# Optimization experiments

Measured on AMD Instinct MI355X. Metric: run time of the kernel, lower is better.

Reference implementation:

```python
import jax, jax.numpy as jnp
import numpy as np

KNN_K = 16
EPS = 1e-5


def _knn_idx(p, k):
    # p: [B,3,N] -> idx [B,N,k] of nearest neighbors (self excluded)
    pt = jnp.swapaxes(p, 1, 2)                      # [B,N,3]
    xx = jnp.sum(pt * pt, axis=-1)                  # [B,N]
    inner = jnp.einsum('bnd,bmd->bnm', pt, pt)      # [B,N,N]
    dist = -(xx[:, :, None] - 2.0 * inner + xx[:, None, :])  # -||pi-pj||^2
    N = pt.shape[1]
    dist = dist - 1e9 * jnp.eye(N, dtype=dist.dtype)
    return jax.lax.top_k(dist, k)[1]


def _ln(x, g, b):
    mu = jnp.mean(x, axis=-1, keepdims=True)
    var = jnp.mean((x - mu) ** 2, axis=-1, keepdims=True)
    return (x - mu) * jax.lax.rsqrt(var + EPS) * g + b


_gather = jax.vmap(lambda a, i: a[i])  # a:[N,C], i:[N,k] -> [N,k,C]


def setup_inputs() -> dict:
    key = jax.random.key(0)
    ks = jax.random.split(key, 24)
    Cin, C, B, N = 64, 128, 8, 2048
    s = lambda k_, shp, fan: jax.random.normal(k_, shp, jnp.float32) * (1.0 / np.sqrt(fan))
    return {
        'x': jax.random.normal(ks[0], (B, Cin, N), jnp.float32),
        'p': jax.random.normal(ks[1], (B, 3, N), jnp.float32),
        'Win': s(ks[2], (C, Cin), Cin), 'bin_': jnp.zeros((C,), jnp.float32),
        'Wq': s(ks[3], (C, C), C), 'Wk': s(ks[4], (C, C), C), 'Wv': s(ks[5], (C, C), C),
        'Wd1': s(ks[6], (C, 3), 3), 'bd1': jnp.zeros((C,), jnp.float32),
        'Wd2': s(ks[7], (C, C), C), 'bd2': jnp.zeros((C,), jnp.float32),
        'Wa': s(ks[8], (C, C), C), 'ba': jnp.zeros((C,), jnp.float32),
        'g1': jnp.ones((C,), jnp.float32), 'b1': jnp.zeros((C,), jnp.float32),
        'g2': jnp.ones((C,), jnp.float32), 'b2': jnp.zeros((C,), jnp.float32),
        'Wf1': s(ks[9], (4 * C, C), C), 'bf1': jnp.zeros((4 * C,), jnp.float32),
        'Wf2': s(ks[10], (C, 4 * C), 4 * C), 'bf2': jnp.zeros((C,), jnp.float32),
    }


def reference(x, p, Win, bin_, Wq, Wk, Wv, Wd1, bd1, Wd2, bd2, Wa, ba,
              g1, b1, g2, b2, Wf1, bf1, Wf2, bf2) -> jnp.ndarray:
    B, _, N = x.shape
    k = min(KNN_K, max(1, N - 1))
    # in_proj (conv1x1 == per-point linear); work in [B,N,C]
    h = jnp.einsum('oc,bcn->bno', Win, x) + bin_          # [B,N,C]
    hn = _ln(h, g1, b1)
    idx = _knn_idx(p, k)                                  # [B,N,k] (int)
    q = hn @ Wq.T                                         # [B,N,C]
    k_all = hn @ Wk.T
    v_all = hn @ Wv.T
    k_j = _gather(k_all, idx)                             # [B,N,k,C]
    v_j = _gather(v_all, idx)
    pt = jnp.swapaxes(p, 1, 2)                            # [B,N,3]
    p_j = _gather(pt, idx)                                # [B,N,k,3]
    rel = pt[:, :, None, :] - p_j                         # [B,N,k,3]
    d = jax.nn.relu(rel @ Wd1.T + bd1) @ Wd2.T + bd2      # [B,N,k,C]
    logits = (q[:, :, None, :] - k_j + d) @ Wa.T + ba     # [B,N,k,C]
    a = jax.nn.softmax(logits, axis=2)                    # softmax over neighbors
    y = jnp.sum(a * (v_j + d), axis=2)                    # [B,N,C]
    h = h + y
    h2 = _ln(h, g2, b2)
    h = h + jax.nn.relu(h2 @ Wf1.T + bf1) @ Wf2.T + bf2
    return jnp.swapaxes(h, 1, 2)                          # [B,C,N]
```

## Files before the change

kernel.cpp:

```cpp
#include <hip/hip_runtime.h>

typedef __bf16 bf16_t;
typedef __bf16 bf16x8 __attribute__((ext_vector_type(8)));
typedef __bf16 bf16x2 __attribute__((ext_vector_type(2)));
typedef float  f32x4  __attribute__((ext_vector_type(4)));

#define MFMA16(a,b,c) __builtin_amdgcn_mfma_f32_16x16x32_bf16((a),(b),(c),0,0,0)

#define BB 8
#define NN 2048
#define CC 128
#define CIN 64
#define KNB 16
#define BNT (BB*NN)

static __device__ __forceinline__ int remap256(int x) { return ((x & 7) << 5) | (x >> 3); }

static __device__ __forceinline__ bf16x8 cvt8(const float* src) {
  f32x4 a0 = *(const f32x4*)src;
  f32x4 a1 = *(const f32x4*)(src + 4);
  bf16x8 fr;
  fr[0] = (__bf16)a0[0]; fr[1] = (__bf16)a0[1]; fr[2] = (__bf16)a0[2]; fr[3] = (__bf16)a0[3];
  fr[4] = (__bf16)a1[0]; fr[5] = (__bf16)a1[1]; fr[6] = (__bf16)a1[2]; fr[7] = (__bf16)a1[3];
  return fr;
}

__global__ __launch_bounds__(256) void inproj_ln_k(
    const float* __restrict__ x, const float* __restrict__ Win, const float* __restrict__ bin,
    const float* __restrict__ g1, const float* __restrict__ b1,
    float* __restrict__ h, bf16_t* __restrict__ hnb) {
  __shared__ bf16_t As[64 * 72];
  __shared__ bf16_t Bs[128 * 72];
  __shared__ float hs[64 * 132];
  int t = threadIdx.x;
  int lane = t & 63, w = t >> 6, quad = lane >> 4, l15 = lane & 15;
  int mBase = remap256(blockIdx.x) * 64;
  int b = mBase >> 11, n0 = mBase & (NN - 1);
  const float* xb = x + (size_t)b * CIN * NN;
  {
    int k = t >> 2, part = t & 3;
    #pragma unroll
    for (int i = 0; i < 4; ++i) {
      f32x4 v = *(const f32x4*)(xb + (size_t)k * NN + n0 + part * 16 + i * 4);
      #pragma unroll
      for (int j2 = 0; j2 < 4; ++j2) As[(part * 16 + i * 4 + j2) * 72 + k] = (__bf16)v[j2];
    }
  }
  {
    int row = t >> 1, seg = (t & 1) * 32;
    #pragma unroll
    for (int i = 0; i < 4; ++i)
      *(bf16x8*)(&Bs[row * 72 + seg + i * 8]) = cvt8(Win + (size_t)row * CIN + seg + i * 8);
  }
  __syncthreads();
  f32x4 acc[2][4] = {};
  #pragma unroll
  for (int s = 0; s < 2; ++s) {
    bf16x8 af[4];
    #pragma unroll
    for (int mt = 0; mt < 4; ++mt)
      af[mt] = *(const bf16x8*)(&As[(mt * 16 + l15) * 72 + s * 32 + quad * 8]);
    #pragma unroll
    for (int t2 = 0; t2 < 2; ++t2) {
      bf16x8 bfr = *(const bf16x8*)(&Bs[((w * 2 + t2) * 16 + l15) * 72 + s * 32 + quad * 8]);
      #pragma unroll
      for (int mt = 0; mt < 4; ++mt) acc[t2][mt] = MFMA16(af[mt], bfr, acc[t2][mt]);
    }
  }
  #pragma unroll
  for (int t2 = 0; t2 < 2; ++t2) {
    int col = (w * 2 + t2) * 16 + l15;
    float bv = bin[col];
    #pragma unroll
    for (int mt = 0; mt < 4; ++mt)
      #pragma unroll
      for (int reg = 0; reg < 4; ++reg)
        hs[(mt * 16 + quad * 4 + reg) * 132 + col] = acc[t2][mt][reg] + bv;
  }
  __syncthreads();
  {
    int row = t >> 2, c0 = (t & 3) * 32;
    float v[32];
    #pragma unroll
    for (int i = 0; i < 8; ++i) *(f32x4*)(v + i * 4) = *(const f32x4*)(&hs[row * 132 + c0 + i * 4]);
    float s1 = 0.f, s2 = 0.f;
    #pragma unroll
    for (int i = 0; i < 32; ++i) { s1 += v[i]; s2 += v[i] * v[i]; }
    s1 += __shfl_xor(s1, 1); s1 += __shfl_xor(s1, 2);
    s2 += __shfl_xor(s2, 1); s2 += __shfl_xor(s2, 2);
    float mu = s1 * (1.f / CC);
    float var = s2 * (1.f / CC) - mu * mu;
    float rs = rsqrtf(var + 1e-5f);
    float* hrow = h + (size_t)(mBase + row) * CC + c0;
    #pragma unroll
    for (int i = 0; i < 8; ++i) *(f32x4*)(hrow + i * 4) = *(const f32x4*)(v + i * 4);
    bf16_t* hnrow = hnb + (size_t)(mBase + row) * CC + c0;
    #pragma unroll
    for (int i = 0; i < 4; ++i) {
      f32x4 g4a = ((const f32x4*)g1)[(c0 >> 2) + i * 2],     g4b = ((const f32x4*)g1)[(c0 >> 2) + i * 2 + 1];
      f32x4 b4a = ((const f32x4*)b1)[(c0 >> 2) + i * 2],     b4b = ((const f32x4*)b1)[(c0 >> 2) + i * 2 + 1];
      bf16x8 o;
      #pragma unroll
      for (int j = 0; j < 4; ++j) o[j]     = (__bf16)((v[i * 8 + j]     - mu) * rs * g4a[j] + b4a[j]);
      #pragma unroll
      for (int j = 0; j < 4; ++j) o[4 + j] = (__bf16)((v[i * 8 + 4 + j] - mu) * rs * g4b[j] + b4b[j]);
      *(bf16x8*)(hnrow + i * 8) = o;
    }
  }
}

static __device__ __forceinline__ void cas(double& a, double& b) {
  double lo = fmin(a, b), hi = fmax(a, b); a = lo; b = hi;
}
#define S8(K,o) \
  cas(K[o+0],K[o+1]); cas(K[o+2],K[o+3]); cas(K[o+4],K[o+5]); cas(K[o+6],K[o+7]); \
  cas(K[o+0],K[o+2]); cas(K[o+1],K[o+3]); cas(K[o+4],K[o+6]); cas(K[o+5],K[o+7]); \
  cas(K[o+1],K[o+2]); cas(K[o+5],K[o+6]); \
  cas(K[o+0],K[o+4]); cas(K[o+1],K[o+5]); cas(K[o+2],K[o+6]); cas(K[o+3],K[o+7]); \
  cas(K[o+2],K[o+4]); cas(K[o+3],K[o+5]); \
  cas(K[o+1],K[o+2]); cas(K[o+3],K[o+4]); cas(K[o+5],K[o+6]);
#define M8(K,a,b) \
  K[a+0]=fmin(K[a+0],K[b+7]); K[a+1]=fmin(K[a+1],K[b+6]); K[a+2]=fmin(K[a+2],K[b+5]); K[a+3]=fmin(K[a+3],K[b+4]); \
  K[a+4]=fmin(K[a+4],K[b+3]); K[a+5]=fmin(K[a+5],K[b+2]); K[a+6]=fmin(K[a+6],K[b+1]); K[a+7]=fmin(K[a+7],K[b+0]); \
  cas(K[a+0],K[a+4]); cas(K[a+1],K[a+5]); cas(K[a+2],K[a+6]); cas(K[a+3],K[a+7]); \
  cas(K[a+0],K[a+2]); cas(K[a+1],K[a+3]); cas(K[a+4],K[a+6]); cas(K[a+5],K[a+7]); \
  cas(K[a+0],K[a+1]); cas(K[a+2],K[a+3]); cas(K[a+4],K[a+5]); cas(K[a+6],K[a+7]);

__global__ __launch_bounds__(256) void knn_k(const float* __restrict__ p, int* __restrict__ idxo) {
  __shared__ float px[NN], py[NN], pz[NN];
  int t = threadIdx.x;
  int b = blockIdx.x >> 9;
  int g = blockIdx.x & 511;
  const float* pb = p + (size_t)b * 3 * NN;
  for (int i = t; i < NN; i += 256) { px[i] = pb[i]; py[i] = pb[NN + i]; pz[i] = pb[2 * NN + i]; }
  __syncthreads();
  int w = t >> 6, lane = t & 63;
  int n = g * 4 + w;
  float pnx = px[n], pny = py[n], pnz = pz[n];
  double key[32];
  #pragma unroll
  for (int s = 0; s < 32; ++s) {
    int m = s * 64 + lane;
    float dx = pnx - px[m], dy = pny - py[m], dz = pnz - pz[m];
    float dist = dx * dx + dy * dy + dz * dz;
    unsigned db = (m == n) ? 0x7F800000u : __float_as_uint(dist);
    key[s] = __hiloint2double((int)db, m);
  }
  S8(key, 0); S8(key, 8); S8(key, 16); S8(key, 24);
  M8(key, 0, 8); M8(key, 16, 24); M8(key, 0, 16);
  const double DINF = __hiloint2double(0x7F900000, 0);
  int* myout = idxo + ((size_t)b * NN + n) * KNB;
  #pragma unroll 1
  for (int r = 0; r < 16; ++r) {
    double gm = key[0];
    #pragma unroll
    for (int off = 1; off < 64; off <<= 1) {
      double o = __shfl_xor(gm, off);
      gm = fmin(gm, o);
    }
    if (lane == 0) myout[r] = __double2loint(gm);
    bool win = (key[0] == gm);
    key[0] = win ? key[1] : key[0];
    key[1] = win ? key[2] : key[1];
    key[2] = win ? key[3] : key[2];
    key[3] = win ? key[4] : key[3];
    key[4] = win ? key[5] : key[4];
    key[5] = win ? key[6] : key[5];
    key[6] = win ? key[7] : key[6];
    key[7] = win ? DINF   : key[7];
  }
}

template<int EPI>
static __device__ __forceinline__ void gemm_body(
    const bf16_t* __restrict__ Ab,
    const float* __restrict__ W, const float* __restrict__ bias,
    float* __restrict__ outF, bf16_t* __restrict__ outB,
    const float* __restrict__ resid,
    int mBase, int nBase, int Ncol, int Kdim) {
  __shared__ bf16_t As[64 * 40];
  __shared__ bf16_t Bs[64 * 40];
  int t = threadIdx.x;
  int lane = t & 63, w = t >> 6, quad = lane >> 4, l15 = lane & 15;
  int r = t >> 2, seg = (t & 3) * 8;
  f32x4 acc[4] = {{0,0,0,0},{0,0,0,0},{0,0,0,0},{0,0,0,0}};
  for (int k0 = 0; k0 < Kdim; k0 += 32) {
    __syncthreads();
    *(bf16x8*)(&As[r * 40 + seg]) = *(const bf16x8*)(Ab + (size_t)(mBase + r) * Kdim + k0 + seg);
    *(bf16x8*)(&Bs[r * 40 + seg]) = cvt8(W + (size_t)(nBase + r) * Kdim + k0 + seg);
    __syncthreads();
    bf16x8 bfr = *(const bf16x8*)(&Bs[(w * 16 + l15) * 40 + quad * 8]);
    #pragma unroll
    for (int mt = 0; mt < 4; ++mt) {
      bf16x8 afr = *(const bf16x8*)(&As[(mt * 16 + l15) * 40 + quad * 8]);
      acc[mt] = MFMA16(afr, bfr, acc[mt]);
    }
  }
  int n = nBase + w * 16 + l15;
  float bv = bias ? bias[n] : 0.f;
  #pragma unroll
  for (int mt = 0; mt < 4; ++mt) {
    #pragma unroll
    for (int reg = 0; reg < 4; ++reg) {
      int m = mBase + mt * 16 + quad * 4 + reg;
      float val = acc[mt][reg] + bv;
      if (EPI == 0) {
        outF[(size_t)m * Ncol + n] = val;
      } else if (EPI == 1) {
        outB[(size_t)m * Ncol + n] = (__bf16)fmaxf(val, 0.f);
      } else if (EPI == 3) {
        outB[(size_t)m * Ncol + n] = (__bf16)val;
      } else {
        val += resid[(size_t)m * CC + n];
        int bo = m >> 11, np = m & (NN - 1);
        outF[((size_t)bo * CC + n) * NN + np] = val;
      }
    }
  }
}

template<int EPI>
__global__ __launch_bounds__(256) void gemm_k(
    const bf16_t* __restrict__ Ab,
    const float* __restrict__ W, const float* __restrict__ bias,
    float* __restrict__ outF, bf16_t* __restrict__ outB,
    const float* __restrict__ resid,
    int Ncol, int Kdim) {
  gemm_body<EPI>(Ab, W, bias, outF, outB, resid, remap256(blockIdx.x) * 64, blockIdx.y * 64, Ncol, Kdim);
}

__global__ __launch_bounds__(256) void gemm_qkv_k(
    const bf16_t* __restrict__ hnb,
    const float* __restrict__ Wq, const float* __restrict__ Wk, const float* __restrict__ Wv,
    float* __restrict__ q, bf16_t* __restrict__ kb, bf16_t* __restrict__ vb) {
  int sel = blockIdx.y >> 1;
  int nB = (blockIdx.y & 1) * 64, mB = remap256(blockIdx.x) * 64;
  if (sel == 0)      gemm_body<0>(hnb, Wq, nullptr, q, nullptr, nullptr, mB, nB, CC, CC);
  else if (sel == 1) gemm_body<3>(hnb, Wk, nullptr, nullptr, kb, nullptr, mB, nB, CC, CC);
  else               gemm_body<3>(hnb, Wv, nullptr, nullptr, vb, nullptr, mB, nB, CC, CC);
}

__global__ __launch_bounds__(256, 3) void attn_k(
    const float* __restrict__ qbuf, const bf16_t* __restrict__ kbuf, const bf16_t* __restrict__ vbuf,
    const float* __restrict__ p, const int* __restrict__ idx,
    const float* __restrict__ Wd1, const float* __restrict__ bd1,
    const float* __restrict__ Wd2, const float* __restrict__ bd2,
    const float* __restrict__ Wa, const float* __restrict__ ba,
    const float* __restrict__ g2, const float* __restrict__ b2,
    const float* __restrict__ h, float* __restrict__ hres, bf16_t* __restrict__ h2) {
  __shared__ bf16_t ts[64 * 136];
  __shared__ float hrs[4 * 128];
  __shared__ f32x4 wd1s[128];
  __shared__ f32x4 rels4[64];
  __shared__ int idxs[64];
  int t = threadIdx.x;
  int lane = t & 63, w = t >> 6, quad = lane >> 4, l15 = lane & 15;
  int batch = blockIdx.x & 7, grp = blockIdx.x >> 3;
  int bn0 = batch * NN + grp * 4;
  int b = batch;
  const float* pb = p + (size_t)b * 3 * NN;
  int col0 = w * 32 + l15;
  int col1 = w * 32 + 16 + l15;

  bf16x8 Bd[2][4];
  #pragma unroll
  for (int t2 = 0; t2 < 2; ++t2) {
    int row = w * 32 + t2 * 16 + l15;
    #pragma unroll
    for (int s = 0; s < 4; ++s)
      Bd[t2][s] = cvt8(Wd2 + (size_t)row * CC + s * 32 + quad * 8);
  }

  if (t < 64) {
    int jj = idx[(size_t)bn0 * KNB + t];
    idxs[t] = jj;
    int npt = grp * 4 + (t >> 4);
    f32x4 rv;
    rv[0] = pb[npt]          - pb[jj];
    rv[1] = pb[NN + npt]     - pb[NN + jj];
    rv[2] = pb[2 * NN + npt] - pb[2 * NN + jj];
    rv[3] = 0.f;
    rels4[t] = rv;
  }
  if (t < 128) {
    f32x4 wv;
    wv[0] = Wd1[t * 3]; wv[1] = Wd1[t * 3 + 1]; wv[2] = Wd1[t * 3 + 2]; wv[3] = bd1[t];
    wd1s[t] = wv;
  }
  __syncthreads();

  float qv[2][4];
  #pragma unroll
  for (int mt = 0; mt < 4; ++mt) {
    qv[0][mt] = qbuf[(size_t)(bn0 + mt) * CC + col0];
    qv[1][mt] = qbuf[(size_t)(bn0 + mt) * CC + col1];
  }
  float kreg[2][4][4];
  #pragma unroll
  for (int mt = 0; mt < 4; ++mt)
    #pragma unroll
    for (int reg = 0; reg < 4; ++reg) {
      size_t base = (size_t)(b * NN + idxs[mt * 16 + quad * 4 + reg]) * CC;
      kreg[0][mt][reg] = (float)kbuf[base + col0];
      kreg[1][mt][reg] = (float)kbuf[base + col1];
    }

  f32x4 relv[4];
  #pragma unroll
  for (int mt = 0; mt < 4; ++mt) relv[mt] = rels4[mt * 16 + l15];
  f32x4 accd[2][4] = {};
  #pragma unroll
  for (int s = 0; s < 4; ++s) {
    bf16x8 af[4];
    #pragma unroll
    for (int j = 0; j < 8; ++j) {
      f32x4 wv = wd1s[s * 32 + quad * 8 + j];
      #pragma unroll
      for (int mt = 0; mt < 4; ++mt) {
        float tv = fmaf(wv[0], relv[mt][0], fmaf(wv[1], relv[mt][1], fmaf(wv[2], relv[mt][2], wv[3])));
        af[mt][j] = (__bf16)fmaxf(tv, 0.f);
      }
    }
    #pragma unroll
    for (int t2 = 0; t2 < 2; ++t2)
      #pragma unroll
      for (int mt = 0; mt < 4; ++mt)
        accd[t2][mt] = MFMA16(af[mt], Bd[t2][s], accd[t2][mt]);
  }

  {
    float b2v0 = bd2[col0], b2v1 = bd2[col1];
    #pragma unroll
    for (int mt = 0; mt < 4; ++mt)
      #pragma unroll
      for (int reg = 0; reg < 4; ++reg) {
        int row = mt * 16 + quad * 4 + reg;
        float d0 = accd[0][mt][reg] + b2v0;
        float d1 = accd[1][mt][reg] + b2v1;
        accd[0][mt][reg] = d0;
        accd[1][mt][reg] = d1;
        ts[row * 136 + col0] = (__bf16)(qv[0][mt] - kreg[0][mt][reg] + d0);
        ts[row * 136 + col1] = (__bf16)(qv[1][mt] - kreg[1][mt][reg] + d1);
      }
  }
  __syncthreads();

  float vreg[2][4][4];
  #pragma unroll
  for (int mt = 0; mt < 4; ++mt)
    #pragma unroll
    for (int reg = 0; reg < 4; ++reg) {
      size_t base = (size_t)(b * NN + idxs[mt * 16 + quad * 4 + reg]) * CC;
      vreg[0][mt][reg] = (float)vbuf[base + col0];
      vreg[1][mt][reg] = (float)vbuf[base + col1];
    }
  float hv[2][4];
  if (quad == 0) {
    #pragma unroll
    for (int mt = 0; mt < 4; ++mt) {
      hv[0][mt] = h[(size_t)(bn0 + mt) * CC + col0];
      hv[1][mt] = h[(size_t)(bn0 + mt) * CC + col1];
    }
  }
  bf16x8 Ba[2][4];
  #pragma unroll
  for (int t2 = 0; t2 < 2; ++t2) {
    int row = w * 32 + t2 * 16 + l15;
    #pragma unroll
    for (int s = 0; s < 4; ++s)
      Ba[t2][s] = cvt8(Wa + (size_t)row * CC + s * 32 + quad * 8);
  }

  f32x4 accl[2][4] = {};
  #pragma unroll
  for (int s = 0; s < 4; ++s) {
    bf16x8 af[4];
    #pragma unroll
    for (int mt = 0; mt < 4; ++mt)
      af[mt] = *(const bf16x8*)(&ts[(mt * 16 + l15) * 136 + s * 32 + quad * 8]);
    #pragma unroll
    for (int t2 = 0; t2 < 2; ++t2)
      #pragma unroll
      for (int mt = 0; mt < 4; ++mt)
        accl[t2][mt] = MFMA16(af[mt], Ba[t2][s], accl[t2][mt]);
  }

  #pragma unroll
  for (int t2 = 0; t2 < 2; ++t2) {
    int col = t2 ? col1 : col0;
    float bav = ba[col];
    #pragma unroll
    for (int mt = 0; mt < 4; ++mt) {
      float lv0 = accl[t2][mt][0] + bav, lv1 = accl[t2][mt][1] + bav;
      float lv2 = accl[t2][mt][2] + bav, lv3 = accl[t2][mt][3] + bav;
      float mx = fmaxf(fmaxf(lv0, lv1), fmaxf(lv2, lv3));
      mx = fmaxf(mx, __shfl_xor(mx, 16));
      mx = fmaxf(mx, __shfl_xor(mx, 32));
      float e0 = __expf(lv0 - mx), e1 = __expf(lv1 - mx);
      float e2 = __expf(lv2 - mx), e3 = __expf(lv3 - mx);
      float ss = e0 + e1 + e2 + e3;
      ss += __shfl_xor(ss, 16); ss += __shfl_xor(ss, 32);
      float yv = e0 * (vreg[t2][mt][0] + accd[t2][mt][0])
               + e1 * (vreg[t2][mt][1] + accd[t2][mt][1])
               + e2 * (vreg[t2][mt][2] + accd[t2][mt][2])
               + e3 * (vreg[t2][mt][3] + accd[t2][mt][3]);
      yv += __shfl_xor(yv, 16); yv += __shfl_xor(yv, 32);
      if (quad == 0) {
        float hvv = hv[t2][mt] + yv / ss;
        hres[(size_t)(bn0 + mt) * CC + col] = hvv;
        hrs[mt * 128 + col] = hvv;
      }
    }
  }
  __syncthreads();

  {
    int c0 = lane * 2;
    float v0 = hrs[w * 128 + c0], v1 = hrs[w * 128 + c0 + 1];
    float s1 = v0 + v1, s2 = v0 * v0 + v1 * v1;
    #pragma unroll
    for (int off = 1; off < 64; off <<= 1) { s1 += __shfl_xor(s1, off); s2 += __shfl_xor(s2, off); }
    float mu = s1 * (1.f / CC);
    float var = s2 * (1.f / CC) - mu * mu;
    float rs = rsqrtf(var + 1e-5f);
    bf16x2 o;
    o[0] = (__bf16)((v0 - mu) * rs * g2[c0] + b2[c0]);
    o[1] = (__bf16)((v1 - mu) * rs * g2[c0 + 1] + b2[c0 + 1]);
    *(bf16x2*)(h2 + (size_t)(bn0 + w) * CC + c0) = o;
  }
}

extern "C" void kernel_launch(void* const* d_in, const int* in_sizes, int n_in,
                              void* d_out, int out_size, void* d_ws, size_t ws_size,
                              hipStream_t stream) {
  const float* x   = (const float*)d_in[0];
  const float* p   = (const float*)d_in[1];
  const float* Win = (const float*)d_in[2];
  const float* bin = (const float*)d_in[3];
  const float* Wq  = (const float*)d_in[4];
  const float* Wk  = (const float*)d_in[5];
  const float* Wv  = (const float*)d_in[6];
  const float* Wd1 = (const float*)d_in[7];
  const float* bd1 = (const float*)d_in[8];
  const float* Wd2 = (const float*)d_in[9];
  const float* bd2 = (const float*)d_in[10];
  const float* Wa  = (const float*)d_in[11];
  const float* ba  = (const float*)d_in[12];
  const float* g1  = (const float*)d_in[13];
  const float* b1  = (const float*)d_in[14];
  const float* g2  = (const float*)d_in[15];
  const float* b2  = (const float*)d_in[16];
  const float* Wf1 = (const float*)d_in[17];
  const float* bf1 = (const float*)d_in[18];
  const float* Wf2 = (const float*)d_in[19];
  const float* bf2 = (const float*)d_in[20];
  float* out = (float*)d_out;

  const size_t SZ = (size_t)BNT * CC;
  float* wsf = (float*)d_ws;
  float*  h    = wsf;
  bf16_t* hnb  = (bf16_t*)(wsf + SZ);
  float*  hres = wsf + SZ;
  float*  q    = wsf + 2 * SZ;
  bf16_t* kb   = (bf16_t*)(wsf + 3 * SZ);
  bf16_t* vb   = kb + SZ;
  bf16_t* g    = (bf16_t*)(wsf + 2 * SZ);
  bf16_t* h2   = (bf16_t*)(wsf + 4 * SZ);
  int*    idxw = (int*)(wsf + 4 * SZ + SZ / 2);

  inproj_ln_k<<<BNT / 64, 256, 0, stream>>>(x, Win, bin, g1, b1, h, hnb);
  knn_k<<<BB * (NN / 4), 256, 0, stream>>>(p, idxw);
  gemm_qkv_k<<<dim3(BNT / 64, 6), 256, 0, stream>>>(hnb, Wq, Wk, Wv, q, kb, vb);
  attn_k<<<BNT / 4, 256, 0, stream>>>(q, kb, vb, p, idxw, Wd1, bd1, Wd2, bd2, Wa, ba,
                                      g2, b2, h, hres, h2);
  gemm_k<1><<<dim3(BNT / 64, 8), 256, 0, stream>>>(h2, Wf1, bf1, nullptr, g, nullptr, 4 * CC, CC);
  gemm_k<2><<<dim3(BNT / 64, 2), 256, 0, stream>>>(g, Wf2, bf2, out, nullptr, hres, CC, 4 * CC);
}
```

Before: 291.8 us.

## Fold Wa into Wq, Wk and Wd2 to remove attention logits GEMM

```diff
diff --git a/kernel.cpp b/kernel.cpp
--- a/kernel.cpp
+++ b/kernel.cpp
@@ -23,6 +23,42 @@
   fr[0] = (__bf16)a0[0]; fr[1] = (__bf16)a0[1]; fr[2] = (__bf16)a0[2]; fr[3] = (__bf16)a0[3];
   fr[4] = (__bf16)a1[0]; fr[5] = (__bf16)a1[1]; fr[6] = (__bf16)a1[2]; fr[7] = (__bf16)a1[3];
   return fr;
+}
+
+__global__ __launch_bounds__(256) void compw_k(
+    const float* __restrict__ Wa, const float* __restrict__ Wq,
+    const float* __restrict__ Wk, const float* __restrict__ Wd2,
+    const float* __restrict__ ba, const float* __restrict__ bd2,
+    float* __restrict__ Waq, float* __restrict__ Wak, float* __restrict__ Wda,
+    float* __restrict__ cb) {
+  __shared__ float Bs[64 * 128];
+  int t = threadIdx.x;
+  int mat = blockIdx.y;
+  const float* B = mat == 0 ? Wq : mat == 1 ? Wk : Wd2;
+  float* O = mat == 0 ? Waq : mat == 1 ? Wak : Wda;
+  int row = blockIdx.x * 16 + (t >> 4);
+  int c0 = (t & 15) * 8;
+  const float* ar = Wa + row * 128;
+  float acc[8] = {};
+  for (int half = 0; half < 2; ++half) {
+    __syncthreads();
+    for (int i = t; i < 64 * 128 / 4; i += 256)
+      ((f32x4*)Bs)[i] = ((const f32x4*)(B + half * 64 * 128))[i];
+    __syncthreads();
+    #pragma unroll 4
+    for (int e = 0; e < 64; ++e) {
+      float av = ar[half * 64 + e];
+      #pragma unroll
+      for (int j = 0; j < 8; ++j) acc[j] = fmaf(av, Bs[e * 128 + c0 + j], acc[j]);
+    }
+  }
+  #pragma unroll
+  for (int j = 0; j < 8; ++j) O[row * 128 + c0 + j] = acc[j];
+  if (mat == 2 && blockIdx.x == 0 && t < 128) {
+    float s = 0.f;
+    for (int e = 0; e < 128; ++e) s = fmaf(Wa[t * 128 + e], bd2[e], s);
+    cb[t] = ba[t] + s;
+  }
 }
 
 __global__ __launch_bounds__(256) void inproj_ln_k(
@@ -231,44 +267,44 @@
 
 __global__ __launch_bounds__(256) void gemm_qkv_k(
     const bf16_t* __restrict__ hnb,
-    const float* __restrict__ Wq, const float* __restrict__ Wk, const float* __restrict__ Wv,
-    float* __restrict__ q, bf16_t* __restrict__ kb, bf16_t* __restrict__ vb) {
+    const float* __restrict__ Waq, const float* __restrict__ Wak, const float* __restrict__ Wv,
+    float* __restrict__ qa, bf16_t* __restrict__ ka, bf16_t* __restrict__ vb) {
   int sel = blockIdx.y >> 1;
   int nB = (blockIdx.y & 1) * 64, mB = remap256(blockIdx.x) * 64;
-  if (sel == 0)      gemm_body<0>(hnb, Wq, nullptr, q, nullptr, nullptr, mB, nB, CC, CC);
-  else if (sel == 1) gemm_body<3>(hnb, Wk, nullptr, nullptr, kb, nullptr, mB, nB, CC, CC);
+  if (sel == 0)      gemm_body<0>(hnb, Waq, nullptr, qa, nullptr, nullptr, mB, nB, CC, CC);
+  else if (sel == 1) gemm_body<3>(hnb, Wak, nullptr, nullptr, ka, nullptr, mB, nB, CC, CC);
   else               gemm_body<3>(hnb, Wv, nullptr, nullptr, vb, nullptr, mB, nB, CC, CC);
 }
 
 __global__ __launch_bounds__(256, 3) void attn_k(
-    const float* __restrict__ qbuf, const bf16_t* __restrict__ kbuf, const bf16_t* __restrict__ vbuf,
+    const float* __restrict__ qabuf, const bf16_t* __restrict__ kabuf, const bf16_t* __restrict__ vbuf,
     const float* __restrict__ p, const int* __restrict__ idx,
     const float* __restrict__ Wd1, const float* __restrict__ bd1,
-    const float* __restrict__ Wd2, const float* __restrict__ bd2,
-    const float* __restrict__ Wa, const float* __restrict__ ba,
+    const float* __restrict__ Wd2, const float* __restrict__ Wda,
+    const float* __restrict__ cb, const float* __restrict__ bd2,
     const float* __restrict__ g2, const float* __restrict__ b2,
     const float* __restrict__ h, float* __restrict__ hres, bf16_t* __restrict__ h2) {
-  __shared__ bf16_t ts[64 * 136];
-  __shared__ float hrs[4 * 128];
   __shared__ f32x4 wd1s[128];
   __shared__ f32x4 rels4[64];
   __shared__ int idxs[64];
+  __shared__ float hrs[4 * 128];
   int t = threadIdx.x;
   int lane = t & 63, w = t >> 6, quad = lane >> 4, l15 = lane & 15;
   int batch = blockIdx.x & 7, grp = blockIdx.x >> 3;
   int bn0 = batch * NN + grp * 4;
-  int b = batch;
-  const float* pb = p + (size_t)b * 3 * NN;
+  const float* pb = p + (size_t)batch * 3 * NN;
   int col0 = w * 32 + l15;
-  int col1 = w * 32 + 16 + l15;
-
-  bf16x8 Bd[2][4];
+  int col1 = col0 + 16;
+
+  bf16x8 Bd[2][4], Bl[2][4];
   #pragma unroll
   for (int t2 = 0; t2 < 2; ++t2) {
     int row = w * 32 + t2 * 16 + l15;
     #pragma unroll
-    for (int s = 0; s < 4; ++s)
+    for (int s = 0; s < 4; ++s) {
       Bd[t2][s] = cvt8(Wd2 + (size_t)row * CC + s * 32 + quad * 8);
+      Bl[t2][s] = cvt8(Wda + (size_t)row * CC + s * 32 + quad * 8);
+    }
   }
 
   if (t < 64) {
@@ -289,26 +325,11 @@
   }
   __syncthreads();
 
-  float qv[2][4];
-  #pragma unroll
-  for (int mt = 0; mt < 4; ++mt) {
-    qv[0][mt] = qbuf[(size_t)(bn0 + mt) * CC + col0];
-    qv[1][mt] = qbuf[(size_t)(bn0 + mt) * CC + col1];
-  }
-  float kreg[2][4][4];
-  #pragma unroll
-  for (int mt = 0; mt < 4; ++mt)
-    #pragma unroll
-    for (int reg = 0; reg < 4; ++reg) {
-      size_t base = (size_t)(b * NN + idxs[mt * 16 + quad * 4 + reg]) * CC;
-      kreg[0][mt][reg] = (float)kbuf[base + col0];
-      kreg[1][mt][reg] = (float)kbuf[base + col1];
-    }
-
   f32x4 relv[4];
   #pragma unroll
   for (int mt = 0; mt < 4; ++mt) relv[mt] = rels4[mt * 16 + l15];
   f32x4 accd[2][4] = {};
+  f32x4 accl[2][4] = {};
   #pragma unroll
   for (int s = 0; s < 4; ++s) {
     bf16x8 af[4];
@@ -324,35 +345,28 @@
     #pragma unroll
     for (int t2 = 0; t2 < 2; ++t2)
       #pragma unroll
-      for (int mt = 0; mt < 4; ++mt)
+      for (int mt = 0; mt < 4; ++mt) {
         accd[t2][mt] = MFMA16(af[mt], Bd[t2][s], accd[t2][mt]);
-  }
-
-  {
-    float b2v0 = bd2[col0], b2v1 = bd2[col1];
-    #pragma unroll
-    for (int mt = 0; mt < 4; ++mt)
-      #pragma unroll
-      for (int reg = 0; reg < 4; ++reg) {
-        int row = mt * 16 + quad * 4 + reg;
-        float d0 = accd[0][mt][reg] + b2v0;
-        float d1 = accd[1][mt][reg] + b2v1;
-        accd[0][mt][reg] = d0;
-        accd[1][mt][reg] = d1;
-        ts[row * 136 + col0] = (__bf16)(qv[0][mt] - kreg[0][mt][reg] + d0);
-        ts[row * 136 + col1] = (__bf16)(qv[1][mt] - kreg[1][mt][reg] + d1);
+        accl[t2][mt] = MFMA16(af[mt], Bl[t2][s], accl[t2][mt]);
       }
   }
-  __syncthreads();
-
-  float vreg[2][4][4];
+
+  float qv[2][4];
+  #pragma unroll
+  for (int mt = 0; mt < 4; ++mt) {
+    qv[0][mt] = qabuf[(size_t)(bn0 + mt) * CC + col0];
+    qv[1][mt] = qabuf[(size_t)(bn0 + mt) * CC + col1];
+  }
+  float kav[2][4][4], vv[2][4][4];
   #pragma unroll
   for (int mt = 0; mt < 4; ++mt)
     #pragma unroll
     for (int reg = 0; reg < 4; ++reg) {
-      size_t base = (size_t)(b * NN + idxs[mt * 16 + quad * 4 + reg]) * CC;
-      vreg[0][mt][reg] = (float)vbuf[base + col0];
-      vreg[1][mt][reg] = (float)vbuf[base + col1];
+      size_t base = (size_t)(batch * NN + idxs[mt * 16 + quad * 4 + reg]) * CC;
+      kav[0][mt][reg] = (float)kabuf[base + col0];
+      kav[1][mt][reg] = (float)kabuf[base + col1];
+      vv[0][mt][reg]  = (float)vbuf[base + col0];
+      vv[1][mt][reg]  = (float)vbuf[base + col1];
     }
   float hv[2][4];
   if (quad == 0) {
@@ -362,37 +376,19 @@
       hv[1][mt] = h[(size_t)(bn0 + mt) * CC + col1];
     }
   }
-  bf16x8 Ba[2][4];
-  #pragma unroll
-  for (int t2 = 0; t2 < 2; ++t2) {
-    int row = w * 32 + t2 * 16 + l15;
-    #pragma unroll
-    for (int s = 0; s < 4; ++s)
-      Ba[t2][s] = cvt8(Wa + (size_t)row * CC + s * 32 + quad * 8);
-  }
-
-  f32x4 accl[2][4] = {};
-  #pragma unroll
-  for (int s = 0; s < 4; ++s) {
-    bf16x8 af[4];
-    #pragma unroll
-    for (int mt = 0; mt < 4; ++mt)
-      af[mt] = *(const bf16x8*)(&ts[(mt * 16 + l15) * 136 + s * 32 + quad * 8]);
-    #pragma unroll
-    for (int t2 = 0; t2 < 2; ++t2)
-      #pragma unroll
-      for (int mt = 0; mt < 4; ++mt)
-        accl[t2][mt] = MFMA16(af[mt], Ba[t2][s], accl[t2][mt]);
-  }
 
   #pragma unroll
   for (int t2 = 0; t2 < 2; ++t2) {
     int col = t2 ? col1 : col0;
-    float bav = ba[col];
+    float cbv = cb[col];
+    float b2v = bd2[col];
     #pragma unroll
     for (int mt = 0; mt < 4; ++mt) {
-      float lv0 = accl[t2][mt][0] + bav, lv1 = accl[t2][mt][1] + bav;
-      float lv2 = accl[t2][mt][2] + bav, lv3 = accl[t2][mt][3] + bav;
+      float qc = qv[t2][mt] + cbv;
+      float lv0 = qc - kav[t2][mt][0] + accl[t2][mt][0];
+      float lv1 = qc - kav[t2][mt][1] + accl[t2][mt][1];
+      float lv2 = qc - kav[t2][mt][2] + accl[t2][mt][2];
+      float lv3 = qc - kav[t2][mt][3] + accl[t2][mt][3];
       float mx = fmaxf(fmaxf(lv0, lv1), fmaxf(lv2, lv3));
       mx = fmaxf(mx, __shfl_xor(mx, 16));
       mx = fmaxf(mx, __shfl_xor(mx, 32));
@@ -400,10 +396,10 @@
       float e2 = __expf(lv2 - mx), e3 = __expf(lv3 - mx);
       float ss = e0 + e1 + e2 + e3;
       ss += __shfl_xor(ss, 16); ss += __shfl_xor(ss, 32);
-      float yv = e0 * (vreg[t2][mt][0] + accd[t2][mt][0])
-               + e1 * (vreg[t2][mt][1] + accd[t2][mt][1])
-               + e2 * (vreg[t2][mt][2] + accd[t2][mt][2])
-               + e3 * (vreg[t2][mt][3] + accd[t2][mt][3]);
+      float yv = e0 * (vv[t2][mt][0] + accd[t2][mt][0] + b2v)
+               + e1 * (vv[t2][mt][1] + accd[t2][mt][1] + b2v)
+               + e2 * (vv[t2][mt][2] + accd[t2][mt][2] + b2v)
+               + e3 * (vv[t2][mt][3] + accd[t2][mt][3] + b2v);
       yv += __shfl_xor(yv, 16); yv += __shfl_xor(yv, 32);
       if (quad == 0) {
         float hvv = hv[t2][mt] + yv / ss;
@@ -461,17 +457,22 @@
   float*  h    = wsf;
   bf16_t* hnb  = (bf16_t*)(wsf + SZ);
   float*  hres = wsf + SZ;
-  float*  q    = wsf + 2 * SZ;
-  bf16_t* kb   = (bf16_t*)(wsf + 3 * SZ);
-  bf16_t* vb   = kb + SZ;
+  float*  qa   = wsf + 2 * SZ;
+  bf16_t* kab  = (bf16_t*)(wsf + 3 * SZ);
+  bf16_t* vb   = kab + SZ;
   bf16_t* g    = (bf16_t*)(wsf + 2 * SZ);
   bf16_t* h2   = (bf16_t*)(wsf + 4 * SZ);
   int*    idxw = (int*)(wsf + 4 * SZ + SZ / 2);
-
+  float*  Waq  = wsf + 4 * SZ + SZ / 2 + (size_t)BNT * KNB;
+  float*  Wak  = Waq + 16384;
+  float*  Wda  = Wak + 16384;
+  float*  cbv  = Wda + 16384;
+
+  compw_k<<<dim3(8, 3), 256, 0, stream>>>(Wa, Wq, Wk, Wd2, ba, bd2, Waq, Wak, Wda, cbv);
   inproj_ln_k<<<BNT / 64, 256, 0, stream>>>(x, Win, bin, g1, b1, h, hnb);
   knn_k<<<BB * (NN / 4), 256, 0, stream>>>(p, idxw);
-  gemm_qkv_k<<<dim3(BNT / 64, 6), 256, 0, stream>>>(hnb, Wq, Wk, Wv, q, kb, vb);
-  attn_k<<<BNT / 4, 256, 0, stream>>>(q, kb, vb, p, idxw, Wd1, bd1, Wd2, bd2, Wa, ba,
+  gemm_qkv_k<<<dim3(BNT / 64, 6), 256, 0, stream>>>(hnb, Waq, Wak, Wv, qa, kab, vb);
+  attn_k<<<BNT / 4, 256, 0, stream>>>(qa, kab, vb, p, idxw, Wd1, bd1, Wd2, Wda, cbv, bd2,
                                       g2, b2, h, hres, h2);
   gemm_k<1><<<dim3(BNT / 64, 8), 256, 0, stream>>>(h2, Wf1, bf1, nullptr, g, nullptr, 4 * CC, CC);
   gemm_k<2><<<dim3(BNT / 64, 2), 256, 0, stream>>>(g, Wf2, bf2, out, nullptr, hres, CC, 4 * CC);
```

Measured after the change: 312.2 us. 1.07x slower.

## Merge KNN and QKV projection into one launch and widen GEMM K-tile

Applied to the files above, without the earlier changes.

```diff
diff --git a/kernel.cpp b/kernel.cpp
--- a/kernel.cpp
+++ b/kernel.cpp
@@ -126,11 +126,12 @@
   cas(K[a+0],K[a+2]); cas(K[a+1],K[a+3]); cas(K[a+4],K[a+6]); cas(K[a+5],K[a+7]); \
   cas(K[a+0],K[a+1]); cas(K[a+2],K[a+3]); cas(K[a+4],K[a+5]); cas(K[a+6],K[a+7]);
 
-__global__ __launch_bounds__(256) void knn_k(const float* __restrict__ p, int* __restrict__ idxo) {
-  __shared__ float px[NN], py[NN], pz[NN];
+static __device__ void knn_impl(float* sp, const float* __restrict__ p,
+                                int* __restrict__ idxo, int bid) {
+  float* px = sp; float* py = sp + NN; float* pz = sp + 2 * NN;
   int t = threadIdx.x;
-  int b = blockIdx.x >> 9;
-  int g = blockIdx.x & 511;
+  int b = bid >> 9;
+  int g = bid & 511;
   const float* pb = p + (size_t)b * 3 * NN;
   for (int i = t; i < NN; i += 256) { px[i] = pb[i]; py[i] = pb[NN + i]; pz[i] = pb[2 * NN + i]; }
   __syncthreads();
@@ -172,28 +173,31 @@
 }
 
 template<int EPI>
-static __device__ __forceinline__ void gemm_body(
-    const bf16_t* __restrict__ Ab,
-    const float* __restrict__ W, const float* __restrict__ bias,
-    float* __restrict__ outF, bf16_t* __restrict__ outB,
-    const float* __restrict__ resid,
+static __device__ void gemm_body2(bf16_t* As, bf16_t* Bs,
+    const bf16_t* __restrict__ Ab, const float* __restrict__ W, const float* __restrict__ bias,
+    float* __restrict__ outF, bf16_t* __restrict__ outB, const float* __restrict__ resid,
     int mBase, int nBase, int Ncol, int Kdim) {
-  __shared__ bf16_t As[64 * 40];
-  __shared__ bf16_t Bs[64 * 40];
   int t = threadIdx.x;
   int lane = t & 63, w = t >> 6, quad = lane >> 4, l15 = lane & 15;
-  int r = t >> 2, seg = (t & 3) * 8;
+  int r = t >> 2, segbase = (t & 3) * 32;
   f32x4 acc[4] = {{0,0,0,0},{0,0,0,0},{0,0,0,0},{0,0,0,0}};
-  for (int k0 = 0; k0 < Kdim; k0 += 32) {
+  for (int k0 = 0; k0 < Kdim; k0 += 128) {
     __syncthreads();
-    *(bf16x8*)(&As[r * 40 + seg]) = *(const bf16x8*)(Ab + (size_t)(mBase + r) * Kdim + k0 + seg);
-    *(bf16x8*)(&Bs[r * 40 + seg]) = cvt8(W + (size_t)(nBase + r) * Kdim + k0 + seg);
+    #pragma unroll
+    for (int i = 0; i < 4; ++i) {
+      int seg = segbase + i * 8;
+      *(bf16x8*)(&As[r * 136 + seg]) = *(const bf16x8*)(Ab + (size_t)(mBase + r) * Kdim + k0 + seg);
+      *(bf16x8*)(&Bs[r * 136 + seg]) = cvt8(W + (size_t)(nBase + r) * Kdim + k0 + seg);
+    }
     __syncthreads();
-    bf16x8 bfr = *(const bf16x8*)(&Bs[(w * 16 + l15) * 40 + quad * 8]);
-    #pragma unroll
-    for (int mt = 0; mt < 4; ++mt) {
-      bf16x8 afr = *(const bf16x8*)(&As[(mt * 16 + l15) * 40 + quad * 8]);
-      acc[mt] = MFMA16(afr, bfr, acc[mt]);
+    #pragma unroll
+    for (int s = 0; s < 4; ++s) {
+      bf16x8 bfr = *(const bf16x8*)(&Bs[(w * 16 + l15) * 136 + s * 32 + quad * 8]);
+      #pragma unroll
+      for (int mt = 0; mt < 4; ++mt) {
+        bf16x8 afr = *(const bf16x8*)(&As[(mt * 16 + l15) * 136 + s * 32 + quad * 8]);
+        acc[mt] = MFMA16(afr, bfr, acc[mt]);
+      }
     }
   }
   int n = nBase + w * 16 + l15;
@@ -221,23 +225,34 @@
 
 template<int EPI>
 __global__ __launch_bounds__(256) void gemm_k(
-    const bf16_t* __restrict__ Ab,
-    const float* __restrict__ W, const float* __restrict__ bias,
-    float* __restrict__ outF, bf16_t* __restrict__ outB,
-    const float* __restrict__ resid,
+    const bf16_t* __restrict__ Ab, const float* __restrict__ W, const float* __restrict__ bias,
+    float* __restrict__ outF, bf16_t* __restrict__ outB, const float* __restrict__ resid,
     int Ncol, int Kdim) {
-  gemm_body<EPI>(Ab, W, bias, outF, outB, resid, remap256(blockIdx.x) * 64, blockIdx.y * 64, Ncol, Kdim);
-}
-
-__global__ __launch_bounds__(256) void gemm_qkv_k(
+  __shared__ bf16_t As[64 * 136];
+  __shared__ bf16_t Bs[64 * 136];
+  gemm_body2<EPI>(As, Bs, Ab, W, bias, outF, outB, resid,
+                  remap256(blockIdx.x) * 64, blockIdx.y * 64, Ncol, Kdim);
+}
+
+__global__ __launch_bounds__(256) void knn_qkv_k(
+    const float* __restrict__ p, int* __restrict__ idxo,
     const bf16_t* __restrict__ hnb,
     const float* __restrict__ Wq, const float* __restrict__ Wk, const float* __restrict__ Wv,
     float* __restrict__ q, bf16_t* __restrict__ kb, bf16_t* __restrict__ vb) {
-  int sel = blockIdx.y >> 1;
-  int nB = (blockIdx.y & 1) * 64, mB = remap256(blockIdx.x) * 64;
-  if (sel == 0)      gemm_body<0>(hnb, Wq, nullptr, q, nullptr, nullptr, mB, nB, CC, CC);
-  else if (sel == 1) gemm_body<3>(hnb, Wk, nullptr, nullptr, kb, nullptr, mB, nB, CC, CC);
-  else               gemm_body<3>(hnb, Wv, nullptr, nullptr, vb, nullptr, mB, nB, CC, CC);
+  __shared__ __align__(16) char smem[2 * 64 * 136 * 2];
+  if (blockIdx.x < 4096) {
+    knn_impl((float*)smem, p, idxo, blockIdx.x);
+  } else {
+    bf16_t* As = (bf16_t*)smem;
+    bf16_t* Bs = As + 64 * 136;
+    int bx = blockIdx.x - 4096;
+    int yy = bx >> 8, xx = bx & 255;
+    int sel = yy >> 1;
+    int mB = remap256(xx) * 64, nB = (yy & 1) * 64;
+    if (sel == 0)      gemm_body2<0>(As, Bs, hnb, Wq, nullptr, q,  nullptr, nullptr, mB, nB, CC, CC);
+    else if (sel == 1) gemm_body2<3>(As, Bs, hnb, Wk, nullptr, nullptr, kb, nullptr, mB, nB, CC, CC);
+    else               gemm_body2<3>(As, Bs, hnb, Wv, nullptr, nullptr, vb, nullptr, mB, nB, CC, CC);
+  }
 }
 
 __global__ __launch_bounds__(256, 3) void attn_k(
@@ -260,7 +275,7 @@
   int b = batch;
   const float* pb = p + (size_t)b * 3 * NN;
   int col0 = w * 32 + l15;
-  int col1 = w * 32 + 16 + l15;
+  int col1 = col0 + 16;
 
   bf16x8 Bd[2][4];
   #pragma unroll
@@ -469,8 +484,7 @@
   int*    idxw = (int*)(wsf + 4 * SZ + SZ / 2);
 
   inproj_ln_k<<<BNT / 64, 256, 0, stream>>>(x, Win, bin, g1, b1, h, hnb);
-  knn_k<<<BB * (NN / 4), 256, 0, stream>>>(p, idxw);
-  gemm_qkv_k<<<dim3(BNT / 64, 6), 256, 0, stream>>>(hnb, Wq, Wk, Wv, q, kb, vb);
+  knn_qkv_k<<<4096 + 1536, 256, 0, stream>>>(p, idxw, hnb, Wq, Wk, Wv, q, kb, vb);
   attn_k<<<BNT / 4, 256, 0, stream>>>(q, kb, vb, p, idxw, Wd1, bd1, Wd2, bd2, Wa, ba,
                                       g2, b2, h, hres, h2);
   gemm_k<1><<<dim3(BNT / 64, 8), 256, 0, stream>>>(h2, Wf1, bf1, nullptr, g, nullptr, 4 * CC, CC);
```

Result: no change. 295.1 us (+1.1%).
